# Optimization experiments

Hardware: AMD Instinct MI355X
Metric: run time of the kernel (lower is better)

Reference implementation:

```python
import jax, jax.numpy as jnp
import numpy as np

N = 40000      # nodes
E = 640000     # edges (avg degree 16)
H = 128        # hidden_dim
D = 4          # propagation_depth
G = 1250       # graphs in batch
T = 32         # target_dim
AF, AV = 9, 64   # atom categorical features, vocab per feature
BF, BV = 3, 8    # bond categorical features, vocab per feature


def silu(x):
    return x * jax.nn.sigmoid(x)


def setup_inputs() -> dict:
    key = jax.random.key(0)
    ks = jax.random.split(key, 32)
    s = 1.0 / np.sqrt(H)

    def w(i, shp, scale):
        return (jax.random.normal(ks[i], shp, jnp.float32) * scale).astype(jnp.float32)

    inp = {}
    inp["atom_feat"] = jax.random.randint(ks[0], (N, AF), 0, AV)
    inp["bond_feat"] = jax.random.randint(ks[1], (E, BF), 0, BV)
    inp["edge_src"] = jax.random.randint(ks[2], (E,), 0, N)
    inp["edge_dst"] = jax.random.randint(ks[3], (E,), 0, N)
    inp["node2graph"] = jnp.sort(jax.random.randint(ks[4], (N,), 0, G))

    inp["atom_emb"] = w(5, (AF, AV, H), 0.1)
    inp["bond_emb"] = w(6, (BF, BV, H), 0.1)
    # message MLP: Linear(3H,H)+SiLU, Linear(H,H)+SiLU (last_activation=mid_activation)
    inp["msg_W1"] = w(7, (D, 3 * H, H), 1.0 / np.sqrt(3 * H))
    inp["msg_b1"] = jnp.zeros((D, H), jnp.float32)
    inp["msg_W2"] = w(8, (D, H, H), s)
    inp["msg_b2"] = jnp.zeros((D, H), jnp.float32)
    # soft edge gate: Linear(H,1) + sigmoid
    inp["gate_W"] = w(9, (D, H, 1), s)
    inp["gate_b"] = jnp.zeros((D, 1), jnp.float32)
    # update MLP: Linear(H,H)+SiLU, Linear(H,H) (last None)
    inp["upd_W1"] = w(10, (D, H, H), s)
    inp["upd_b1"] = jnp.zeros((D, H), jnp.float32)
    inp["upd_W2"] = w(11, (D, H, H), s)
    inp["upd_b2"] = jnp.zeros((D, H), jnp.float32)
    # node_wise_output: Linear(H,H)+SiLU, Linear(H,H) (last None)
    inp["out_W1"] = w(12, (H, H), s)
    inp["out_b1"] = jnp.zeros((H,), jnp.float32)
    inp["out_W2"] = w(13, (H, H), s)
    inp["out_b2"] = jnp.zeros((H,), jnp.float32)
    # readout output MLP: Linear(3H,H)+ReLU, Linear(H,T) (last None)
    inp["ro_W1"] = w(14, (3 * H, H), 1.0 / np.sqrt(3 * H))
    inp["ro_b1"] = jnp.zeros((H,), jnp.float32)
    inp["ro_W2"] = w(15, (H, T), s)
    inp["ro_b2"] = jnp.zeros((T,), jnp.float32)
    return inp


def _forward(atom_feat, bond_feat, edge_src, edge_dst, node2graph,
             atom_emb, bond_emb,
             msg_W1, msg_b1, msg_W2, msg_b2, gate_W, gate_b,
             upd_W1, upd_b1, upd_W2, upd_b2,
             out_W1, out_b1, out_W2, out_b2,
             ro_W1, ro_b1, ro_W2, ro_b2):
    # Atom/Bond encoders: sum of per-feature categorical embeddings
    h = atom_emb[jnp.arange(AF), atom_feat].sum(axis=1)        # [N, H]
    e = bond_emb[jnp.arange(BF), bond_feat].sum(axis=1)        # [E, H]

    for l in range(D):
        src = h[edge_src]                                      # [E, H]
        dst = h[edge_dst]                                      # [E, H]
        m_in = jnp.concatenate([src, dst, e], axis=-1)         # [E, 3H]
        m = silu(silu(m_in @ msg_W1[l] + msg_b1[l]) @ msg_W2[l] + msg_b2[l])
        gate = jax.nn.sigmoid(m @ gate_W[l] + gate_b[l])       # [E, 1]
        m = m * gate
        m_sum = jax.ops.segment_sum(m, edge_dst, num_segments=N)  # [N, H]
        u_in = m_sum + h
        h_new = silu(u_in @ upd_W1[l] + upd_b1[l]) @ upd_W2[l] + upd_b2[l]
        h = h_new + h

    # node-wise output network
    h = silu(h @ out_W1 + out_b1) @ out_W2 + out_b2            # [N, H]

    # per-graph readouts: sum / mean / max
    sums = jax.ops.segment_sum(h, node2graph, num_segments=G)  # [G, H]
    cnt = jax.ops.segment_sum(jnp.ones((N, 1), h.dtype), node2graph, num_segments=G)
    mean = sums / jnp.maximum(cnt, 1.0)
    mx = jax.ops.segment_max(h, node2graph, num_segments=G)
    mx = jnp.where(cnt > 0, mx, 0.0)
    readout = jnp.concatenate([sums, mean, mx], axis=-1)       # [G, 3H]

    return jax.nn.relu(readout @ ro_W1 + ro_b1) @ ro_W2 + ro_b2  # [G, T]


def reference(atom_feat, bond_feat, edge_src, edge_dst, node2graph,
              atom_emb, bond_emb,
              msg_W1, msg_b1, msg_W2, msg_b2, gate_W, gate_b,
              upd_W1, upd_b1, upd_W2, upd_b2,
              out_W1, out_b1, out_W2, out_b2,
              ro_W1, ro_b1, ro_W2, ro_b2):
    return _forward(atom_feat, bond_feat, edge_src, edge_dst, node2graph,
                    atom_emb, bond_emb,
                    msg_W1, msg_b1, msg_W2, msg_b2, gate_W, gate_b,
                    upd_W1, upd_b1, upd_W2, upd_b2,
                    out_W1, out_b1, out_W2, out_b2,
                    ro_W1, ro_b1, ro_W2, ro_b2)
```

## Files before the change

kernel.cpp:

```cpp
#include <hip/hip_runtime.h>
#include <hip/hip_bf16.h>

#define NN 40000
#define NE 640000
#define HD 128
#define DEPTH 4
#define NG 1250
#define TD 32
#define AFN 9
#define AVN 64
#define BFN 3
#define BVN 8
#define NBLK (NE / 64)

typedef short bf16x8 __attribute__((ext_vector_type(8)));
typedef float f32x4 __attribute__((ext_vector_type(4)));

__device__ __forceinline__ uint cvtpk(float lo, float hi){
  uint r; asm("v_cvt_pk_bf16_f32 %0, %1, %2" : "=v"(r) : "v"(lo), "v"(hi)); return r;
}
__device__ __forceinline__ ushort f2bf(float x){
  return (ushort)cvtpk(x, x);
}
__device__ __forceinline__ float bf2f(ushort b){ return __uint_as_float(((uint)b) << 16); }
__device__ __forceinline__ float lo16f(uint w){ return __uint_as_float(w << 16); }
__device__ __forceinline__ float hi16f(uint w){ return __uint_as_float(w & 0xffff0000u); }
__device__ __forceinline__ float rcpfa(float x){ return __builtin_amdgcn_rcpf(x); }
__device__ __forceinline__ float siluf(float x){ return x * rcpfa(1.f + __expf(-x)); }
__device__ __forceinline__ float sigmf(float x){ return rcpfa(1.f + __expf(-x)); }
__device__ __forceinline__ uint packbf2(float a, float b){ return cvtpk(a, b); }

__global__ void pack_w(const float* __restrict__ src, ushort* __restrict__ dst,
                       int K, int N, int L){
  int total = L * K * N;
  for (int idx = blockIdx.x * blockDim.x + threadIdx.x; idx < total;
       idx += gridDim.x * blockDim.x){
    int l = idx / (K * N);
    int r = idx - l * K * N;
    int k = r / N;
    int n = r - k * N;
    dst[(size_t)l * K * N + ((size_t)(k >> 3) * N + n) * 8 + (k & 7)] = f2bf(src[idx]);
  }
}

__global__ void zero_f(float4* __restrict__ p, int n4){
  for (int i = blockIdx.x * blockDim.x + threadIdx.x; i < n4; i += gridDim.x * blockDim.x)
    p[i] = make_float4(0.f, 0.f, 0.f, 0.f);
}

__global__ void zero_i(int* __restrict__ p, int n){
  for (int i = blockIdx.x * blockDim.x + threadIdx.x; i < n; i += gridDim.x * blockDim.x)
    p[i] = 0;
}

__global__ void atom_encode(const int* __restrict__ feat, const float* __restrict__ emb,
                            float* __restrict__ h, ushort* __restrict__ hbf){
  int n = blockIdx.x;
  int c = threadIdx.x;
  float acc = 0.f;
#pragma unroll
  for (int f = 0; f < AFN; ++f){
    int v = feat[n * AFN + f];
    acc += emb[(size_t)(f * AVN + v) * HD + c];
  }
  h[(size_t)n * HD + c] = acc;
  hbf[(size_t)n * HD + c] = f2bf(acc);
}

__global__ void ebf_k(const float* __restrict__ bemb, ushort* __restrict__ ebf){
  const int cid = blockIdx.x;
  const int c = threadIdx.x;
  const int f0 = cid >> 6, f1 = (cid >> 3) & 7, f2 = cid & 7;
  float v = bemb[(size_t)(0 * BVN + f0) * HD + c]
          + bemb[(size_t)(1 * BVN + f1) * HD + c]
          + bemb[(size_t)(2 * BVN + f2) * HD + c];
  ebf[(size_t)cid * HD + c] = f2bf(v);
}

__global__ void hist_k(const int* __restrict__ edst, int* __restrict__ deg){
  for (int e = blockIdx.x * blockDim.x + threadIdx.x; e < NE; e += gridDim.x * blockDim.x)
    atomicAdd(&deg[edst[e]], 1);
}

__global__ __launch_bounds__(1024) void scan_head(const int* __restrict__ deg,
                                                  int* __restrict__ head){
  __shared__ int buf[1024];
  const int t = threadIdx.x;
  const int base = t * 40;
  int s = 0;
  int dloc[40];
  if (t < 1000){
#pragma unroll
    for (int i = 0; i < 40; ++i){ dloc[i] = deg[base + i]; s += dloc[i]; }
  }
  buf[t] = s;
  __syncthreads();
  for (int ofs = 1; ofs < 1024; ofs <<= 1){
    int x = (t >= ofs) ? buf[t - ofs] : 0;
    __syncthreads();
    buf[t] += x;
    __syncthreads();
  }
  if (t < 1000){
    int run = buf[t] - s;
#pragma unroll
    for (int i = 0; i < 40; ++i){ head[base + i] = run; run += dloc[i]; }
  }
}

__global__ void scatter_k(const int* __restrict__ esrc, const int* __restrict__ edst,
                          const int* __restrict__ bfeat, int* __restrict__ head,
                          int* __restrict__ esrc_p, int* __restrict__ dst_p,
                          int* __restrict__ cid_p){
  for (int e = blockIdx.x * blockDim.x + threadIdx.x; e < NE; e += gridDim.x * blockDim.x){
    const int d = edst[e];
    const int pos = atomicAdd(&head[d], 1);
    esrc_p[pos] = esrc[e];
    dst_p[pos] = d;
    cid_p[pos] = bfeat[e * 3 + 0] * 64 + bfeat[e * 3 + 1] * 8 + bfeat[e * 3 + 2];
  }
}

__global__ __launch_bounds__(256) void pre_k(
    const ushort* __restrict__ hbf, const ushort* __restrict__ W1p,
    ushort* __restrict__ prea, ushort* __restrict__ preb)
{
  const int tid = threadIdx.x;
  const int n0 = blockIdx.x * 64;
  const int lane = tid & 63, wv = tid >> 6;
  const int lr = lane & 15, lg = lane >> 4;
  const int arow = n0 + wv * 16 + lr;
  bf16x8 a[4];
#pragma unroll
  for (int ks = 0; ks < 4; ++ks)
    a[ks] = *(const bf16x8*)(hbf + (size_t)arow * HD + ks * 32 + lg * 8);
  const f32x4 zero = {0.f, 0.f, 0.f, 0.f};
  f32x4 acc[16];
#pragma unroll
  for (int i = 0; i < 16; ++i) acc[i] = zero;
#pragma unroll
  for (int ks = 0; ks < 4; ++ks){
#pragma unroll
    for (int ct = 0; ct < 16; ++ct){
      const int oct = ks * 4 + lg + ((ct >= 8) ? 16 : 0);
      const int ncol = (ct & 7) * 16 + lr;
      bf16x8 b = *(const bf16x8*)(W1p + ((size_t)oct * HD + ncol) * 8);
      acc[ct] = __builtin_amdgcn_mfma_f32_16x16x32_bf16(a[ks], b, acc[ct], 0, 0, 0);
    }
  }
#pragma unroll
  for (int ct = 0; ct < 16; ++ct){
    ushort* dstp = (ct < 8) ? prea : preb;
    const int ncol = (ct & 7) * 16 + lr;
#pragma unroll
    for (int r = 0; r < 4; ++r){
      const int nrow = n0 + wv * 16 + lg * 4 + r;
      dstp[(size_t)nrow * HD + ncol] = f2bf(acc[ct][r]);
    }
  }
}

__global__ __launch_bounds__(256) void ew1c_k(
    const ushort* __restrict__ ebf, const ushort* __restrict__ W1p_all,
    const float* __restrict__ b1_all, ushort* __restrict__ ecb_all)
{
  const int l = blockIdx.y;
  const ushort* W1p = W1p_all + (size_t)l * 384 * HD;
  const float* b1v = b1_all + l * HD;
  ushort* ecb = ecb_all + (size_t)l * 512 * HD;
  const int tid = threadIdx.x;
  const int c0 = blockIdx.x * 64;
  const int lane = tid & 63, wv = tid >> 6;
  const int lr = lane & 15, lg = lane >> 4;
  const int arow = c0 + wv * 16 + lr;
  bf16x8 a[4];
#pragma unroll
  for (int ks = 0; ks < 4; ++ks)
    a[ks] = *(const bf16x8*)(ebf + (size_t)arow * HD + ks * 32 + lg * 8);
  const f32x4 zero = {0.f, 0.f, 0.f, 0.f};
  f32x4 acc[8];
#pragma unroll
  for (int i = 0; i < 8; ++i) acc[i] = zero;
#pragma unroll
  for (int ks = 0; ks < 4; ++ks){
#pragma unroll
    for (int ct = 0; ct < 8; ++ct){
      const int oct = ks * 4 + lg + 32;
      const int ncol = ct * 16 + lr;
      bf16x8 b = *(const bf16x8*)(W1p + ((size_t)oct * HD + ncol) * 8);
      acc[ct] = __builtin_amdgcn_mfma_f32_16x16x32_bf16(a[ks], b, acc[ct], 0, 0, 0);
    }
  }
#pragma unroll
  for (int ct = 0; ct < 8; ++ct){
    const int ncol = ct * 16 + lr;
    const float bias = b1v[ncol];
#pragma unroll
    for (int r = 0; r < 4; ++r){
      const int nrow = c0 + wv * 16 + lg * 4 + r;
      ecb[(size_t)nrow * HD + ncol] = f2bf(acc[ct][r] + bias);
    }
  }
}

__global__ __launch_bounds__(256, 4) void msg2_kernel(
    const ushort* __restrict__ prea, const ushort* __restrict__ preb,
    const ushort* __restrict__ ecb,
    const int* __restrict__ esrc_p, const int* __restrict__ dst_p,
    const int* __restrict__ cid_p,
    const ushort* __restrict__ W2p, const float* __restrict__ b2v,
    const float* __restrict__ gw, const float* __restrict__ gb,
    float* __restrict__ msum)
{
  __shared__ float Ms[64 * 128];
  __shared__ int dsh[64];
  const int tid = threadIdx.x;
  const int bid = (int)blockIdx.x;
  const int bsw = (bid & 7) * (NBLK >> 3) + (bid >> 3);
  const int e0 = bsw * 64;
  if (tid < 64) dsh[tid] = dst_p[e0 + tid];

  const int lane = tid & 63;
  const int wv = tid >> 6;
  const int lr = lane & 15, lg = lane >> 4;
  const int row = e0 + wv * 16 + lr;
  const int s = esrc_p[row];
  const int d = dst_p[row];
  const int c = cid_p[row];

  bf16x8 af[4];
#pragma unroll
  for (int ks = 0; ks < 4; ++ks){
    const int off = ks * 32 + lg * 8;
    union { bf16x8 v; uint u[4]; } ua, ub, uc, uo;
    ua.v = *(const bf16x8*)(prea + (size_t)s * HD + off);
    ub.v = *(const bf16x8*)(preb + (size_t)d * HD + off);
    uc.v = *(const bf16x8*)(ecb + (size_t)c * HD + off);
#pragma unroll
    for (int j = 0; j < 4; ++j){
      float xl = lo16f(ua.u[j]) + lo16f(ub.u[j]) + lo16f(uc.u[j]);
      float xh = hi16f(ua.u[j]) + hi16f(ub.u[j]) + hi16f(uc.u[j]);
      uo.u[j] = cvtpk(siluf(xl), siluf(xh));
    }
    af[ks] = uo.v;
  }

  const f32x4 zero = {0.f, 0.f, 0.f, 0.f};
  f32x4 acc[8];
#pragma unroll
  for (int i = 0; i < 8; ++i) acc[i] = zero;
#pragma unroll
  for (int ks = 0; ks < 4; ++ks){
    const ushort* wb = W2p + ((size_t)(ks * 4 + lg) * HD + lr) * 8;
#pragma unroll
    for (int ct = 0; ct < 8; ++ct){
      bf16x8 b = *(const bf16x8*)(wb + ct * 16 * 8);
      acc[ct] = __builtin_amdgcn_mfma_f32_16x16x32_bf16(af[ks], b, acc[ct], 0, 0, 0);
    }
  }

  float m[8][4];
#pragma unroll
  for (int ct = 0; ct < 8; ++ct){
    const float bias = b2v[ct * 16 + lr];
#pragma unroll
    for (int r = 0; r < 4; ++r) m[ct][r] = siluf(acc[ct][r] + bias);
  }
  float gwv[8];
#pragma unroll
  for (int ct = 0; ct < 8; ++ct) gwv[ct] = gw[ct * 16 + lr];
  const float gbias = gb[0];
#pragma unroll
  for (int r = 0; r < 4; ++r){
    float sgs = 0.f;
#pragma unroll
    for (int ct = 0; ct < 8; ++ct) sgs += m[ct][r] * gwv[ct];
    sgs += __shfl_xor(sgs, 1); sgs += __shfl_xor(sgs, 2);
    sgs += __shfl_xor(sgs, 4); sgs += __shfl_xor(sgs, 8);
    const float gate = sigmf(sgs + gbias);
#pragma unroll
    for (int ct = 0; ct < 8; ++ct) m[ct][r] *= gate;
  }

#pragma unroll
  for (int ct = 0; ct < 8; ++ct){
    const int col = ct * 16 + lr;
#pragma unroll
    for (int r = 0; r < 4; ++r){
      const int lrow = wv * 16 + lg * 4 + r;
      *(float*)((char*)Ms + lrow * 512 + (((uint)(col * 4)) ^ ((uint)((lrow & 7) << 4)))) = m[ct][r];
    }
  }
  __syncthreads();

  {
    const int col = tid & 127;
    const int seg = tid >> 7;
    const int r0 = seg * 32, r1 = r0 + 32;
    float run = 0.f;
    int cur = dsh[r0];
    for (int r = r0; r < r1; ++r){
      const int dd = dsh[r];
      if (dd != cur){
        atomicAdd(&msum[(size_t)cur * HD + col], run);
        run = 0.f; cur = dd;
      }
      run += *(const float*)((const char*)Ms + r * 512 +
                             (((uint)(col * 4)) ^ ((uint)((r & 7) << 4))));
    }
    atomicAdd(&msum[(size_t)cur * HD + col], run);
  }
}

template <int MODE>
__global__ __launch_bounds__(256) void node_mlp(
    const float* hin, const float* __restrict__ msum,
    const ushort* __restrict__ W1p, const ushort* __restrict__ W2p,
    const float* __restrict__ b1v, const float* __restrict__ b2v,
    float* outp, ushort* __restrict__ hbf)
{
  __shared__ ushort At[64 * 128];
  __shared__ ushort Tt[64 * 128];
  const int tid = threadIdx.x;
  const int n0 = blockIdx.x * 64;

  {
    const int nl = tid >> 2, part = tid & 3;
    const int node = n0 + nl;
    const float4* hp = (const float4*)(hin + (size_t)node * HD + part * 32);
    const float4* mp = (MODE == 0) ? (const float4*)(msum + (size_t)node * HD + part * 32) : nullptr;
    char* rowp = (char*)At + nl * 256;
    const uint sw = (uint)((nl & 7) << 4);
#pragma unroll
    for (int j = 0; j < 4; ++j){
      float4 x0 = hp[j * 2 + 0], x1 = hp[j * 2 + 1];
      if (MODE == 0){
        float4 m0 = mp[j * 2 + 0], m1 = mp[j * 2 + 1];
        x0.x += m0.x; x0.y += m0.y; x0.z += m0.z; x0.w += m0.w;
        x1.x += m1.x; x1.y += m1.y; x1.z += m1.z; x1.w += m1.w;
      }
      uint4 o;
      o.x = packbf2(x0.x, x0.y); o.y = packbf2(x0.z, x0.w);
      o.z = packbf2(x1.x, x1.y); o.w = packbf2(x1.z, x1.w);
      uint cb = (uint)(part * 64 + j * 16);
      *(uint4*)(rowp + (cb ^ sw)) = o;
    }
  }
  __syncthreads();

  const int lane = tid & 63;
  const int wv = tid >> 6;
  const int lr = lane & 15, lg = lane >> 4;
  const int rowbase = wv * 16;
  const f32x4 zero = {0.f, 0.f, 0.f, 0.f};

  f32x4 acc[8];
#pragma unroll
  for (int i = 0; i < 8; ++i) acc[i] = zero;
  {
    const int arow = rowbase + lr;
    const char* arp = (const char*)At + arow * 256;
    const uint asw = (uint)((arow & 7) << 4);
#pragma unroll
    for (int ks = 0; ks < 4; ++ks){
      uint cb = (uint)(ks * 64 + lg * 16);
      bf16x8 a = *(const bf16x8*)(arp + (cb ^ asw));
      const ushort* wbase = W1p + ((size_t)(ks * 4 + lg) * 128 + lr) * 8;
#pragma unroll
      for (int ct = 0; ct < 8; ++ct){
        bf16x8 b = *(const bf16x8*)(wbase + ct * 16 * 8);
        acc[ct] = __builtin_amdgcn_mfma_f32_16x16x32_bf16(a, b, acc[ct], 0, 0, 0);
      }
    }
  }
#pragma unroll
  for (int ct = 0; ct < 8; ++ct){
    const int col = ct * 16 + lr;
    const float bias = b1v[col];
#pragma unroll
    for (int r = 0; r < 4; ++r){
      const int row = rowbase + lg * 4 + r;
      float v = siluf(acc[ct][r] + bias);
      *(ushort*)((char*)Tt + row * 256 + (((uint)(col * 2)) ^ ((uint)(row & 7) << 4))) = f2bf(v);
    }
  }
  __syncthreads();

  f32x4 acc2[8];
#pragma unroll
  for (int i = 0; i < 8; ++i) acc2[i] = zero;
  {
    const int arow = rowbase + lr;
    const char* arp = (const char*)Tt + arow * 256;
    const uint asw = (uint)((arow & 7) << 4);
#pragma unroll
    for (int ks = 0; ks < 4; ++ks){
      uint cb = (uint)(ks * 64 + lg * 16);
      bf16x8 a = *(const bf16x8*)(arp + (cb ^ asw));
      const ushort* wbase = W2p + ((size_t)(ks * 4 + lg) * 128 + lr) * 8;
#pragma unroll
      for (int ct = 0; ct < 8; ++ct){
        bf16x8 b = *(const bf16x8*)(wbase + ct * 16 * 8);
        acc2[ct] = __builtin_amdgcn_mfma_f32_16x16x32_bf16(a, b, acc2[ct], 0, 0, 0);
      }
    }
  }
#pragma unroll
  for (int ct = 0; ct < 8; ++ct){
    const int col = ct * 16 + lr;
    const float bias = b2v[col];
#pragma unroll
    for (int r = 0; r < 4; ++r){
      const int node = n0 + rowbase + lg * 4 + r;
      float v = acc2[ct][r] + bias;
      if (MODE == 0) v += hin[(size_t)node * HD + col];
      outp[(size_t)node * HD + col] = v;
      if (MODE == 0) hbf[(size_t)node * HD + col] = f2bf(v);
    }
  }
}

__global__ void readout_k(const float* __restrict__ hout, const int* __restrict__ n2g,
                          float* __restrict__ ro){
  const int g = blockIdx.x;
  const int c = threadIdx.x;
  int lo, hi;
  { int a = 0, b = NN; while (a < b){ int mid = (a + b) >> 1; if (n2g[mid] < g) a = mid + 1; else b = mid; } lo = a; }
  { int a = lo, b = NN; while (a < b){ int mid = (a + b) >> 1; if (n2g[mid] < g + 1) a = mid + 1; else b = mid; } hi = a; }
  float s = 0.f, mx = -3.4e38f;
  for (int n = lo; n < hi; ++n){
    float v = hout[(size_t)n * HD + c];
    s += v; mx = fmaxf(mx, v);
  }
  const int cnt = hi - lo;
  float mean = (cnt > 0) ? s / (float)cnt : 0.f;
  if (cnt == 0){ s = 0.f; mx = 0.f; }
  ro[(size_t)g * 384 + c] = s;
  ro[(size_t)g * 384 + 128 + c] = mean;
  ro[(size_t)g * 384 + 256 + c] = mx;
}

__global__ void final_k(const float* __restrict__ ro,
                        const float* __restrict__ W1, const float* __restrict__ b1,
                        const float* __restrict__ W2, const float* __restrict__ b2,
                        float* __restrict__ out){
  __shared__ float rsh[384];
  __shared__ float hr[128];
  const int g = blockIdx.x;
  const int t = threadIdx.x;
  for (int i = t; i < 384; i += 128) rsh[i] = ro[(size_t)g * 384 + i];
  __syncthreads();
  float acc = b1[t];
#pragma unroll 4
  for (int j = 0; j < 384; ++j) acc += rsh[j] * W1[j * 128 + t];
  hr[t] = fmaxf(acc, 0.f);
  __syncthreads();
  if (t < TD){
    float o = b2[t];
#pragma unroll 4
    for (int j = 0; j < 128; ++j) o += hr[j] * W2[j * TD + t];
    out[(size_t)g * TD + t] = o;
  }
}

extern "C" void kernel_launch(void* const* d_in, const int* in_sizes, int n_in,
                              void* d_out, int out_size, void* d_ws, size_t ws_size,
                              hipStream_t stream)
{
  const int*   atom_feat  = (const int*)  d_in[0];
  const int*   bond_feat  = (const int*)  d_in[1];
  const int*   edge_src   = (const int*)  d_in[2];
  const int*   edge_dst   = (const int*)  d_in[3];
  const int*   node2graph = (const int*)  d_in[4];
  const float* atom_emb   = (const float*)d_in[5];
  const float* bond_emb   = (const float*)d_in[6];
  const float* msg_W1     = (const float*)d_in[7];
  const float* msg_b1     = (const float*)d_in[8];
  const float* msg_W2     = (const float*)d_in[9];
  const float* msg_b2     = (const float*)d_in[10];
  const float* gate_W     = (const float*)d_in[11];
  const float* gate_b     = (const float*)d_in[12];
  const float* upd_W1     = (const float*)d_in[13];
  const float* upd_b1     = (const float*)d_in[14];
  const float* upd_W2     = (const float*)d_in[15];
  const float* upd_b2     = (const float*)d_in[16];
  const float* out_W1     = (const float*)d_in[17];
  const float* out_b1     = (const float*)d_in[18];
  const float* out_W2     = (const float*)d_in[19];
  const float* out_b2     = (const float*)d_in[20];
  const float* ro_W1      = (const float*)d_in[21];
  const float* ro_b1      = (const float*)d_in[22];
  const float* ro_W2      = (const float*)d_in[23];
  const float* ro_b2      = (const float*)d_in[24];
  (void)in_sizes; (void)n_in; (void)out_size; (void)ws_size;

  char* ws = (char*)d_ws;
  size_t off = 0;
  auto alloc = [&](size_t bytes) -> char* {
    char* p = ws + off;
    off = (off + bytes + 255) & ~(size_t)255;
    return p;
  };
  float*  h      = (float*) alloc((size_t)NN * HD * 4);
  ushort* hbf    = (ushort*)alloc((size_t)NN * HD * 2);
  float*  msum   = (float*) alloc((size_t)NN * HD * 4);
  float*  ro     = (float*) alloc((size_t)NG * 3 * HD * 4);
  ushort* msgW1p = (ushort*)alloc((size_t)DEPTH * 384 * HD * 2);
  ushort* msgW2p = (ushort*)alloc((size_t)DEPTH * HD * HD * 2);
  ushort* updW1p = (ushort*)alloc((size_t)DEPTH * HD * HD * 2);
  ushort* updW2p = (ushort*)alloc((size_t)DEPTH * HD * HD * 2);
  ushort* outW1p = (ushort*)alloc((size_t)HD * HD * 2);
  ushort* outW2p = (ushort*)alloc((size_t)HD * HD * 2);
  ushort* ebf    = (ushort*)alloc((size_t)512 * HD * 2);
  ushort* ecb    = (ushort*)alloc((size_t)DEPTH * 512 * HD * 2);
  ushort* prea   = (ushort*)alloc((size_t)NN * HD * 2);
  ushort* preb   = (ushort*)alloc((size_t)NN * HD * 2);
  int*    deg    = (int*)   alloc((size_t)NN * 4);
  int*    head   = (int*)   alloc((size_t)NN * 4);
  int*    esrc_p = (int*)   alloc((size_t)NE * 4);
  int*    dst_p  = (int*)   alloc((size_t)NE * 4);
  int*    cid_p  = (int*)   alloc((size_t)NE * 4);
  float*  hout   = msum;

  pack_w<<<192, 256, 0, stream>>>(msg_W1, msgW1p, 384, HD, DEPTH);
  pack_w<<<64, 256, 0, stream>>>(msg_W2, msgW2p, HD, HD, DEPTH);
  pack_w<<<64, 256, 0, stream>>>(upd_W1, updW1p, HD, HD, DEPTH);
  pack_w<<<64, 256, 0, stream>>>(upd_W2, updW2p, HD, HD, DEPTH);
  pack_w<<<32, 256, 0, stream>>>(out_W1, outW1p, HD, HD, 1);
  pack_w<<<32, 256, 0, stream>>>(out_W2, outW2p, HD, HD, 1);
  atom_encode<<<NN, HD, 0, stream>>>(atom_feat, atom_emb, h, hbf);
  ebf_k<<<512, HD, 0, stream>>>(bond_emb, ebf);
  ew1c_k<<<dim3(8, DEPTH), 256, 0, stream>>>(ebf, msgW1p, msg_b1, ecb);

  zero_i<<<160, 256, 0, stream>>>(deg, NN);
  hist_k<<<640, 256, 0, stream>>>(edge_dst, deg);
  scan_head<<<1, 1024, 0, stream>>>(deg, head);
  scatter_k<<<640, 256, 0, stream>>>(edge_src, edge_dst, bond_feat, head,
                                     esrc_p, dst_p, cid_p);

  for (int l = 0; l < DEPTH; ++l){
    pre_k<<<NN / 64, 256, 0, stream>>>(hbf, msgW1p + (size_t)l * 384 * HD, prea, preb);
    zero_f<<<1024, 256, 0, stream>>>((float4*)msum, NN * HD / 4);
    msg2_kernel<<<NBLK, 256, 0, stream>>>(
        prea, preb, ecb + (size_t)l * 512 * HD,
        esrc_p, dst_p, cid_p,
        msgW2p + (size_t)l * HD * HD,
        msg_b2 + l * HD, gate_W + l * HD, gate_b + l, msum);
    node_mlp<0><<<NN / 64, 256, 0, stream>>>(
        h, msum,
        updW1p + (size_t)l * HD * HD, updW2p + (size_t)l * HD * HD,
        upd_b1 + l * HD, upd_b2 + l * HD, h, hbf);
  }
  node_mlp<1><<<NN / 64, 256, 0, stream>>>(
      h, nullptr, outW1p, outW2p, out_b1, out_b2, hout, nullptr);
  readout_k<<<NG, HD, 0, stream>>>(hout, node2graph, ro);
  final_k<<<NG, HD, 0, stream>>>(ro, ro_W1, ro_b1, ro_W2, ro_b2, (float*)d_out);
}
```

Baseline: 785.6 us.

## Switch message path to fp16 with packed half math and fuse small kernels

Switches the edge message path (prea/preb/ecb intermediates, W2 weights and the MFMA) from bf16 to fp16. It uses packed half2 SiLU, fdot2 for the gate and a half-sized shared-memory staging buffer, and raises the occupancy hint to 6. It also merges msum zeroing into pre_k, merges the six weight-pack launches into one, and fuses readout with the final MLP. Together these cut ALU work, LDS footprint and launch count, but fp16 range and precision could hurt accuracy on large activations.

```diff
diff --git a/kernel.cpp b/kernel.cpp
--- a/kernel.cpp
+++ b/kernel.cpp
@@ -1,5 +1,6 @@
 #include <hip/hip_runtime.h>
 #include <hip/hip_bf16.h>
+#include <hip/hip_fp16.h>
 
 #define NN 40000
 #define NE 640000
@@ -14,38 +15,56 @@
 #define NBLK (NE / 64)
 
 typedef short bf16x8 __attribute__((ext_vector_type(8)));
+typedef _Float16 f16x8 __attribute__((ext_vector_type(8)));
+typedef _Float16 f16x2 __attribute__((ext_vector_type(2)));
 typedef float f32x4 __attribute__((ext_vector_type(4)));
 
 __device__ __forceinline__ uint cvtpk(float lo, float hi){
   uint r; asm("v_cvt_pk_bf16_f32 %0, %1, %2" : "=v"(r) : "v"(lo), "v"(hi)); return r;
 }
-__device__ __forceinline__ ushort f2bf(float x){
-  return (ushort)cvtpk(x, x);
-}
-__device__ __forceinline__ float bf2f(ushort b){ return __uint_as_float(((uint)b) << 16); }
-__device__ __forceinline__ float lo16f(uint w){ return __uint_as_float(w << 16); }
-__device__ __forceinline__ float hi16f(uint w){ return __uint_as_float(w & 0xffff0000u); }
+__device__ __forceinline__ ushort f2bf(float x){ return (ushort)cvtpk(x, x); }
 __device__ __forceinline__ float rcpfa(float x){ return __builtin_amdgcn_rcpf(x); }
 __device__ __forceinline__ float siluf(float x){ return x * rcpfa(1.f + __expf(-x)); }
 __device__ __forceinline__ float sigmf(float x){ return rcpfa(1.f + __expf(-x)); }
 __device__ __forceinline__ uint packbf2(float a, float b){ return cvtpk(a, b); }
 
-__global__ void pack_w(const float* __restrict__ src, ushort* __restrict__ dst,
-                       int K, int N, int L){
-  int total = L * K * N;
+__device__ __forceinline__ __half2 silu_h2(__half2 x){
+  const __half2 nl2e = __float2half2_rn(-1.44269504f);
+  const __half2 one  = __float2half2_rn(1.f);
+  __half2 e = h2exp2(__hmul2(x, nl2e));
+  return __hmul2(x, h2rcp(__hadd2(one, e)));
+}
+union H2U { __half2 h; f16x2 v; uint u; };
+
+__device__ __forceinline__ void pack_one(const float* __restrict__ src,
+                                         ushort* __restrict__ dst,
+                                         int K, int L, int isf16){
+  int total = L * K * HD;
   for (int idx = blockIdx.x * blockDim.x + threadIdx.x; idx < total;
        idx += gridDim.x * blockDim.x){
-    int l = idx / (K * N);
-    int r = idx - l * K * N;
-    int k = r / N;
-    int n = r - k * N;
-    dst[(size_t)l * K * N + ((size_t)(k >> 3) * N + n) * 8 + (k & 7)] = f2bf(src[idx]);
-  }
-}
-
-__global__ void zero_f(float4* __restrict__ p, int n4){
-  for (int i = blockIdx.x * blockDim.x + threadIdx.x; i < n4; i += gridDim.x * blockDim.x)
-    p[i] = make_float4(0.f, 0.f, 0.f, 0.f);
+    int l = idx / (K * HD);
+    int r = idx - l * K * HD;
+    int k = r / HD;
+    int n = r - k * HD;
+    float v = src[idx];
+    ushort o;
+    if (isf16){ __half hv = __float2half_rn(v); o = *(ushort*)&hv; }
+    else o = f2bf(v);
+    dst[(size_t)l * K * HD + ((size_t)(k >> 3) * HD + n) * 8 + (k & 7)] = o;
+  }
+}
+__global__ void pack6(const float* s0, const float* s1, const float* s2,
+                      const float* s3, const float* s4, const float* s5,
+                      ushort* d0, ushort* d1, ushort* d2,
+                      ushort* d3, ushort* d4, ushort* d5){
+  switch (blockIdx.y){
+    case 0: pack_one(s0, d0, 384, DEPTH, 0); break;
+    case 1: pack_one(s1, d1, HD, DEPTH, 1); break;
+    case 2: pack_one(s2, d2, HD, DEPTH, 0); break;
+    case 3: pack_one(s3, d3, HD, DEPTH, 0); break;
+    case 4: pack_one(s4, d4, HD, 1, 0); break;
+    default: pack_one(s5, d5, HD, 1, 0); break;
+  }
 }
 
 __global__ void zero_i(int* __restrict__ p, int n){
@@ -123,10 +142,17 @@
 
 __global__ __launch_bounds__(256) void pre_k(
     const ushort* __restrict__ hbf, const ushort* __restrict__ W1p,
-    ushort* __restrict__ prea, ushort* __restrict__ preb)
+    __half* __restrict__ prea, __half* __restrict__ preb,
+    float* __restrict__ msum)
 {
   const int tid = threadIdx.x;
   const int n0 = blockIdx.x * 64;
+  {
+    const float4 z = make_float4(0.f, 0.f, 0.f, 0.f);
+    float4* mz = (float4*)(msum + (size_t)n0 * HD);
+#pragma unroll
+    for (int i = 0; i < 8; ++i) mz[tid + i * 256] = z;
+  }
   const int lane = tid & 63, wv = tid >> 6;
   const int lr = lane & 15, lg = lane >> 4;
   const int arow = n0 + wv * 16 + lr;
@@ -150,24 +176,24 @@
   }
 #pragma unroll
   for (int ct = 0; ct < 16; ++ct){
-    ushort* dstp = (ct < 8) ? prea : preb;
+    __half* dstp = (ct < 8) ? prea : preb;
     const int ncol = (ct & 7) * 16 + lr;
 #pragma unroll
     for (int r = 0; r < 4; ++r){
       const int nrow = n0 + wv * 16 + lg * 4 + r;
-      dstp[(size_t)nrow * HD + ncol] = f2bf(acc[ct][r]);
+      dstp[(size_t)nrow * HD + ncol] = __float2half_rn(acc[ct][r]);
     }
   }
 }
 
 __global__ __launch_bounds__(256) void ew1c_k(
     const ushort* __restrict__ ebf, const ushort* __restrict__ W1p_all,
-    const float* __restrict__ b1_all, ushort* __restrict__ ecb_all)
+    const float* __restrict__ b1_all, __half* __restrict__ ecb_all)
 {
   const int l = blockIdx.y;
   const ushort* W1p = W1p_all + (size_t)l * 384 * HD;
   const float* b1v = b1_all + l * HD;
-  ushort* ecb = ecb_all + (size_t)l * 512 * HD;
+  __half* ecb = ecb_all + (size_t)l * 512 * HD;
   const int tid = threadIdx.x;
   const int c0 = blockIdx.x * 64;
   const int lane = tid & 63, wv = tid >> 6;
@@ -198,21 +224,21 @@
 #pragma unroll
     for (int r = 0; r < 4; ++r){
       const int nrow = c0 + wv * 16 + lg * 4 + r;
-      ecb[(size_t)nrow * HD + ncol] = f2bf(acc[ct][r] + bias);
-    }
-  }
-}
-
-__global__ __launch_bounds__(256, 4) void msg2_kernel(
-    const ushort* __restrict__ prea, const ushort* __restrict__ preb,
-    const ushort* __restrict__ ecb,
+      ecb[(size_t)nrow * HD + ncol] = __float2half_rn(acc[ct][r] + bias);
+    }
+  }
+}
+
+__global__ __launch_bounds__(256, 6) void msg2_kernel(
+    const __half* __restrict__ prea, const __half* __restrict__ preb,
+    const __half* __restrict__ ecb,
     const int* __restrict__ esrc_p, const int* __restrict__ dst_p,
     const int* __restrict__ cid_p,
-    const ushort* __restrict__ W2p, const float* __restrict__ b2v,
+    const __half* __restrict__ W2p, const float* __restrict__ b2v,
     const float* __restrict__ gw, const float* __restrict__ gb,
     float* __restrict__ msum)
 {
-  __shared__ float Ms[64 * 128];
+  __shared__ uint Ms[64 * 64];
   __shared__ int dsh[64];
   const int tid = threadIdx.x;
   const int bid = (int)blockIdx.x;
@@ -228,20 +254,17 @@
   const int d = dst_p[row];
   const int c = cid_p[row];
 
-  bf16x8 af[4];
+  f16x8 af[4];
 #pragma unroll
   for (int ks = 0; ks < 4; ++ks){
     const int off = ks * 32 + lg * 8;
-    union { bf16x8 v; uint u[4]; } ua, ub, uc, uo;
-    ua.v = *(const bf16x8*)(prea + (size_t)s * HD + off);
-    ub.v = *(const bf16x8*)(preb + (size_t)d * HD + off);
-    uc.v = *(const bf16x8*)(ecb + (size_t)c * HD + off);
-#pragma unroll
-    for (int j = 0; j < 4; ++j){
-      float xl = lo16f(ua.u[j]) + lo16f(ub.u[j]) + lo16f(uc.u[j]);
-      float xh = hi16f(ua.u[j]) + hi16f(ub.u[j]) + hi16f(uc.u[j]);
-      uo.u[j] = cvtpk(siluf(xl), siluf(xh));
-    }
+    union { uint4 q; __half2 h[4]; f16x8 v; } ua, ub, uc, uo;
+    ua.q = *(const uint4*)(prea + (size_t)s * HD + off);
+    ub.q = *(const uint4*)(preb + (size_t)d * HD + off);
+    uc.q = *(const uint4*)(ecb + (size_t)c * HD + off);
+#pragma unroll
+    for (int j = 0; j < 4; ++j)
+      uo.h[j] = silu_h2(__hadd2(__hadd2(ua.h[j], ub.h[j]), uc.h[j]));
     af[ks] = uo.v;
   }
 
@@ -251,64 +274,79 @@
   for (int i = 0; i < 8; ++i) acc[i] = zero;
 #pragma unroll
   for (int ks = 0; ks < 4; ++ks){
-    const ushort* wb = W2p + ((size_t)(ks * 4 + lg) * HD + lr) * 8;
+    const __half* wb = W2p + ((size_t)(ks * 4 + lg) * HD + lr) * 8;
 #pragma unroll
     for (int ct = 0; ct < 8; ++ct){
-      bf16x8 b = *(const bf16x8*)(wb + ct * 16 * 8);
-      acc[ct] = __builtin_amdgcn_mfma_f32_16x16x32_bf16(af[ks], b, acc[ct], 0, 0, 0);
-    }
-  }
-
-  float m[8][4];
-#pragma unroll
-  for (int ct = 0; ct < 8; ++ct){
-    const float bias = b2v[ct * 16 + lr];
-#pragma unroll
-    for (int r = 0; r < 4; ++r) m[ct][r] = siluf(acc[ct][r] + bias);
-  }
-  float gwv[8];
-#pragma unroll
-  for (int ct = 0; ct < 8; ++ct) gwv[ct] = gw[ct * 16 + lr];
+      f16x8 b = *(const f16x8*)(wb + ct * 16 * 8);
+      acc[ct] = __builtin_amdgcn_mfma_f32_16x16x32_f16(af[ks], b, acc[ct], 0, 0, 0);
+    }
+  }
+
+  float b2l[4], b2h[4];
+  __half2 gwh[4];
+#pragma unroll
+  for (int ct = 0; ct < 4; ++ct){
+    b2l[ct] = b2v[ct * 16 + lr];
+    b2h[ct] = b2v[ct * 16 + lr + 64];
+    gwh[ct] = __floats2half2_rn(gw[ct * 16 + lr], gw[ct * 16 + lr + 64]);
+  }
+  __half2 mh[4][4];
+#pragma unroll
+  for (int ct = 0; ct < 4; ++ct){
+#pragma unroll
+    for (int r = 0; r < 4; ++r){
+      __half2 x = __floats2half2_rn(acc[ct][r] + b2l[ct], acc[ct + 4][r] + b2h[ct]);
+      mh[ct][r] = silu_h2(x);
+    }
+  }
   const float gbias = gb[0];
 #pragma unroll
   for (int r = 0; r < 4; ++r){
     float sgs = 0.f;
 #pragma unroll
-    for (int ct = 0; ct < 8; ++ct) sgs += m[ct][r] * gwv[ct];
+    for (int ct = 0; ct < 4; ++ct){
+      H2U a, b; a.h = mh[ct][r]; b.h = gwh[ct];
+      sgs = __builtin_amdgcn_fdot2(a.v, b.v, sgs, false);
+    }
     sgs += __shfl_xor(sgs, 1); sgs += __shfl_xor(sgs, 2);
     sgs += __shfl_xor(sgs, 4); sgs += __shfl_xor(sgs, 8);
-    const float gate = sigmf(sgs + gbias);
-#pragma unroll
-    for (int ct = 0; ct < 8; ++ct) m[ct][r] *= gate;
-  }
-
-#pragma unroll
-  for (int ct = 0; ct < 8; ++ct){
-    const int col = ct * 16 + lr;
+    const __half2 gh = __float2half2_rn(sigmf(sgs + gbias));
+#pragma unroll
+    for (int ct = 0; ct < 4; ++ct) mh[ct][r] = __hmul2(mh[ct][r], gh);
+  }
+
+#pragma unroll
+  for (int ct = 0; ct < 4; ++ct){
+    const int ui = ct * 16 + lr;
 #pragma unroll
     for (int r = 0; r < 4; ++r){
       const int lrow = wv * 16 + lg * 4 + r;
-      *(float*)((char*)Ms + lrow * 512 + (((uint)(col * 4)) ^ ((uint)((lrow & 7) << 4)))) = m[ct][r];
+      H2U w; w.h = mh[ct][r];
+      *(uint*)((char*)Ms + lrow * 256 + (((uint)(ui * 4)) ^ ((uint)((lrow & 7) << 4)))) = w.u;
     }
   }
   __syncthreads();
 
   {
-    const int col = tid & 127;
-    const int seg = tid >> 7;
-    const int r0 = seg * 32, r1 = r0 + 32;
-    float run = 0.f;
+    const int cp = tid & 63;
+    const int seg = tid >> 6;
+    const int r0 = seg * 16, r1 = r0 + 16;
+    float rl = 0.f, rh = 0.f;
     int cur = dsh[r0];
     for (int r = r0; r < r1; ++r){
       const int dd = dsh[r];
       if (dd != cur){
-        atomicAdd(&msum[(size_t)cur * HD + col], run);
-        run = 0.f; cur = dd;
+        atomicAdd(&msum[(size_t)cur * HD + cp], rl);
+        atomicAdd(&msum[(size_t)cur * HD + cp + 64], rh);
+        rl = 0.f; rh = 0.f; cur = dd;
       }
-      run += *(const float*)((const char*)Ms + r * 512 +
-                             (((uint)(col * 4)) ^ ((uint)((r & 7) << 4))));
-    }
-    atomicAdd(&msum[(size_t)cur * HD + col], run);
+      H2U w;
+      w.u = *(const uint*)((const char*)Ms + r * 256 +
+                           (((uint)(cp * 4)) ^ ((uint)((r & 7) << 4))));
+      rl += __low2float(w.h); rh += __high2float(w.h);
+    }
+    atomicAdd(&msum[(size_t)cur * HD + cp], rl);
+    atomicAdd(&msum[(size_t)cur * HD + cp + 64], rh);
   }
 }
 
@@ -353,24 +391,22 @@
   const int lr = lane & 15, lg = lane >> 4;
   const int rowbase = wv * 16;
   const f32x4 zero = {0.f, 0.f, 0.f, 0.f};
+  const int arow = rowbase + lr;
+  const char* arp = (const char*)At + arow * 256;
+  const uint asw = (uint)((arow & 7) << 4);
 
   f32x4 acc[8];
 #pragma unroll
   for (int i = 0; i < 8; ++i) acc[i] = zero;
-  {
-    const int arow = rowbase + lr;
-    const char* arp = (const char*)At + arow * 256;
-    const uint asw = (uint)((arow & 7) << 4);
-#pragma unroll
-    for (int ks = 0; ks < 4; ++ks){
-      uint cb = (uint)(ks * 64 + lg * 16);
-      bf16x8 a = *(const bf16x8*)(arp + (cb ^ asw));
-      const ushort* wbase = W1p + ((size_t)(ks * 4 + lg) * 128 + lr) * 8;
-#pragma unroll
-      for (int ct = 0; ct < 8; ++ct){
-        bf16x8 b = *(const bf16x8*)(wbase + ct * 16 * 8);
-        acc[ct] = __builtin_amdgcn_mfma_f32_16x16x32_bf16(a, b, acc[ct], 0, 0, 0);
-      }
+#pragma unroll
+  for (int ks = 0; ks < 4; ++ks){
+    uint cb = (uint)(ks * 64 + lg * 16);
+    bf16x8 a = *(const bf16x8*)(arp + (cb ^ asw));
+    const ushort* wbase = W1p + ((size_t)(ks * 4 + lg) * 128 + lr) * 8;
+#pragma unroll
+    for (int ct = 0; ct < 8; ++ct){
+      bf16x8 b = *(const bf16x8*)(wbase + ct * 16 * 8);
+      acc[ct] = __builtin_amdgcn_mfma_f32_16x16x32_bf16(a, b, acc[ct], 0, 0, 0);
     }
   }
 #pragma unroll
@@ -390,13 +426,11 @@
 #pragma unroll
   for (int i = 0; i < 8; ++i) acc2[i] = zero;
   {
-    const int arow = rowbase + lr;
-    const char* arp = (const char*)Tt + arow * 256;
-    const uint asw = (uint)((arow & 7) << 4);
+    const char* trp = (const char*)Tt + arow * 256;
 #pragma unroll
     for (int ks = 0; ks < 4; ++ks){
       uint cb = (uint)(ks * 64 + lg * 16);
-      bf16x8 a = *(const bf16x8*)(arp + (cb ^ asw));
+      bf16x8 a = *(const bf16x8*)(trp + (cb ^ asw));
       const ushort* wbase = W2p + ((size_t)(ks * 4 + lg) * 128 + lr) * 8;
 #pragma unroll
       for (int ct = 0; ct < 8; ++ct){
@@ -420,8 +454,13 @@
   }
 }
 
-__global__ void readout_k(const float* __restrict__ hout, const int* __restrict__ n2g,
-                          float* __restrict__ ro){
+__global__ __launch_bounds__(128) void readout_final(
+    const float* __restrict__ hout, const int* __restrict__ n2g,
+    const float* __restrict__ W1, const float* __restrict__ b1,
+    const float* __restrict__ W2, const float* __restrict__ b2,
+    float* __restrict__ out){
+  __shared__ float rsh[384];
+  __shared__ float hr[128];
   const int g = blockIdx.x;
   const int c = threadIdx.x;
   int lo, hi;
@@ -435,31 +474,18 @@
   const int cnt = hi - lo;
   float mean = (cnt > 0) ? s / (float)cnt : 0.f;
   if (cnt == 0){ s = 0.f; mx = 0.f; }
-  ro[(size_t)g * 384 + c] = s;
-  ro[(size_t)g * 384 + 128 + c] = mean;
-  ro[(size_t)g * 384 + 256 + c] = mx;
-}
-
-__global__ void final_k(const float* __restrict__ ro,
-                        const float* __restrict__ W1, const float* __restrict__ b1,
-                        const float* __restrict__ W2, const float* __restrict__ b2,
-                        float* __restrict__ out){
-  __shared__ float rsh[384];
-  __shared__ float hr[128];
-  const int g = blockIdx.x;
-  const int t = threadIdx.x;
-  for (int i = t; i < 384; i += 128) rsh[i] = ro[(size_t)g * 384 + i];
+  rsh[c] = s; rsh[128 + c] = mean; rsh[256 + c] = mx;
   __syncthreads();
-  float acc = b1[t];
+  float acc = b1[c];
 #pragma unroll 4
-  for (int j = 0; j < 384; ++j) acc += rsh[j] * W1[j * 128 + t];
-  hr[t] = fmaxf(acc, 0.f);
+  for (int j = 0; j < 384; ++j) acc += rsh[j] * W1[j * 128 + c];
+  hr[c] = fmaxf(acc, 0.f);
   __syncthreads();
-  if (t < TD){
-    float o = b2[t];
+  if (c < TD){
+    float o = b2[c];
 #pragma unroll 4
-    for (int j = 0; j < 128; ++j) o += hr[j] * W2[j * TD + t];
-    out[(size_t)g * TD + t] = o;
+    for (int j = 0; j < 128; ++j) o += hr[j] * W2[j * TD + c];
+    out[(size_t)g * TD + c] = o;
   }
 }
 
@@ -504,7 +530,6 @@
   float*  h      = (float*) alloc((size_t)NN * HD * 4);
   ushort* hbf    = (ushort*)alloc((size_t)NN * HD * 2);
   float*  msum   = (float*) alloc((size_t)NN * HD * 4);
-  float*  ro     = (float*) alloc((size_t)NG * 3 * HD * 4);
   ushort* msgW1p = (ushort*)alloc((size_t)DEPTH * 384 * HD * 2);
   ushort* msgW2p = (ushort*)alloc((size_t)DEPTH * HD * HD * 2);
   ushort* updW1p = (ushort*)alloc((size_t)DEPTH * HD * HD * 2);
@@ -512,9 +537,9 @@
   ushort* outW1p = (ushort*)alloc((size_t)HD * HD * 2);
   ushort* outW2p = (ushort*)alloc((size_t)HD * HD * 2);
   ushort* ebf    = (ushort*)alloc((size_t)512 * HD * 2);
-  ushort* ecb    = (ushort*)alloc((size_t)DEPTH * 512 * HD * 2);
-  ushort* prea   = (ushort*)alloc((size_t)NN * HD * 2);
-  ushort* preb   = (ushort*)alloc((size_t)NN * HD * 2);
+  __half* ecb    = (__half*)alloc((size_t)DEPTH * 512 * HD * 2);
+  __half* prea   = (__half*)alloc((size_t)NN * HD * 2);
+  __half* preb   = (__half*)alloc((size_t)NN * HD * 2);
   int*    deg    = (int*)   alloc((size_t)NN * 4);
   int*    head   = (int*)   alloc((size_t)NN * 4);
   int*    esrc_p = (int*)   alloc((size_t)NE * 4);
@@ -522,12 +547,8 @@
   int*    cid_p  = (int*)   alloc((size_t)NE * 4);
   float*  hout   = msum;
 
-  pack_w<<<192, 256, 0, stream>>>(msg_W1, msgW1p, 384, HD, DEPTH);
-  pack_w<<<64, 256, 0, stream>>>(msg_W2, msgW2p, HD, HD, DEPTH);
-  pack_w<<<64, 256, 0, stream>>>(upd_W1, updW1p, HD, HD, DEPTH);
-  pack_w<<<64, 256, 0, stream>>>(upd_W2, updW2p, HD, HD, DEPTH);
-  pack_w<<<32, 256, 0, stream>>>(out_W1, outW1p, HD, HD, 1);
-  pack_w<<<32, 256, 0, stream>>>(out_W2, outW2p, HD, HD, 1);
+  pack6<<<dim3(48, 6), 256, 0, stream>>>(msg_W1, msg_W2, upd_W1, upd_W2, out_W1, out_W2,
+                                         msgW1p, msgW2p, updW1p, updW2p, outW1p, outW2p);
   atom_encode<<<NN, HD, 0, stream>>>(atom_feat, atom_emb, h, hbf);
   ebf_k<<<512, HD, 0, stream>>>(bond_emb, ebf);
   ew1c_k<<<dim3(8, DEPTH), 256, 0, stream>>>(ebf, msgW1p, msg_b1, ecb);
@@ -539,12 +560,11 @@
                                      esrc_p, dst_p, cid_p);
 
   for (int l = 0; l < DEPTH; ++l){
-    pre_k<<<NN / 64, 256, 0, stream>>>(hbf, msgW1p + (size_t)l * 384 * HD, prea, preb);
-    zero_f<<<1024, 256, 0, stream>>>((float4*)msum, NN * HD / 4);
+    pre_k<<<NN / 64, 256, 0, stream>>>(hbf, msgW1p + (size_t)l * 384 * HD, prea, preb, msum);
     msg2_kernel<<<NBLK, 256, 0, stream>>>(
         prea, preb, ecb + (size_t)l * 512 * HD,
         esrc_p, dst_p, cid_p,
-        msgW2p + (size_t)l * HD * HD,
+        (const __half*)msgW2p + (size_t)l * HD * HD,
         msg_b2 + l * HD, gate_W + l * HD, gate_b + l, msum);
     node_mlp<0><<<NN / 64, 256, 0, stream>>>(
         h, msum,
@@ -553,6 +573,6 @@
   }
   node_mlp<1><<<NN / 64, 256, 0, stream>>>(
       h, nullptr, outW1p, outW2p, out_b1, out_b2, hout, nullptr);
-  readout_k<<<NG, HD, 0, stream>>>(hout, node2graph, ro);
-  final_k<<<NG, HD, 0, stream>>>(ro, ro_W1, ro_b1, ro_W2, ro_b2, (float*)d_out);
-}
+  readout_final<<<NG, 128, 0, stream>>>(hout, node2graph, ro_W1, ro_b1, ro_W2, ro_b2,
+                                        (float*)d_out);
+}
```

Result: faster. 767.5 us (-2.3%).
